# Optimization experiments

Hardware: AMD Instinct MI355X
Metric: run time of the kernel (lower is better)

Reference implementation:

```python
import jax, jax.numpy as jnp
import numpy as np
from jax import lax

B, T, D = 4, 1024, 512      # batch, seq_len, d_model
L = 4                        # n_layers
N = 16                       # d_state
DC = 4                       # d_conv
DI = 2 * D                   # d_inner = expand * d_model
DTR = D // 16                # dt_rank
H = 128                      # head hidden dim
EPS = 1e-5


def layer_norm(x, g, b):
    mu = jnp.mean(x, axis=-1, keepdims=True)
    var = jnp.mean((x - mu) ** 2, axis=-1, keepdims=True)
    return (x - mu) * lax.rsqrt(var + EPS) * g + b


def setup_inputs() -> dict:
    key = jax.random.key(0)
    ks = jax.random.split(key, 24)
    s = 0.02
    return {
        "daily_summaries": jax.random.normal(ks[0], (B, T, D), jnp.float32),
        # per-layer mamba params, stacked on leading L axis
        "in_proj_w": s * jax.random.normal(ks[1], (L, 2 * DI, D), jnp.float32),
        "conv_w": s * jax.random.normal(ks[2], (L, DI, DC), jnp.float32),
        "conv_b": jnp.zeros((L, DI), jnp.float32),
        "x_proj_w": s * jax.random.normal(ks[3], (L, DTR + 2 * N, DI), jnp.float32),
        "dt_proj_w": s * jax.random.normal(ks[4], (L, DI, DTR), jnp.float32),
        "dt_proj_b": jnp.full((L, DI), -4.0, jnp.float32),  # softplus -> small dt
        "A_log": jnp.log(jnp.broadcast_to(jnp.arange(1, N + 1, dtype=jnp.float32), (L, DI, N))),
        "D_skip": jnp.ones((L, DI), jnp.float32),
        "out_proj_w": s * jax.random.normal(ks[5], (L, D, DI), jnp.float32),
        "ln_g": jnp.ones((L, D), jnp.float32),
        "ln_b": jnp.zeros((L, D), jnp.float32),
        # attention pooling
        "attn_w": s * jax.random.normal(ks[6], (1, D), jnp.float32),
        "attn_b": jnp.zeros((1,), jnp.float32),
        # VIX head
        "h1_w": s * jax.random.normal(ks[7], (H, D), jnp.float32),
        "h1_b": jnp.zeros((H,), jnp.float32),
        "ln1_g": jnp.ones((H,), jnp.float32),
        "ln1_b": jnp.zeros((H,), jnp.float32),
        "h2_w": s * jax.random.normal(ks[8], (H, H), jnp.float32),
        "h2_b": jnp.zeros((H,), jnp.float32),
        "ln2_g": jnp.ones((H,), jnp.float32),
        "ln2_b": jnp.zeros((H,), jnp.float32),
        # note: torch zero-inits the final layer; we use random so grads are nonzero
        "h3_w": s * jax.random.normal(ks[9], (1, H), jnp.float32),
        "h3_b": jnp.zeros((1,), jnp.float32),
    }


def mamba_layer(x, in_w, cw, cb, xp_w, dt_w, dt_b, A_log, D_skip, out_w):
    """x: [B,T,D] -> [B,T,D]; canonical Mamba selective scan."""
    xz = jnp.einsum('btd,ed->bte', x, in_w)          # [B,T,2*DI]
    x_in, z = jnp.split(xz, 2, axis=-1)
    # causal depthwise conv over time
    xc = lax.conv_general_dilated(
        x_in.transpose(0, 2, 1), cw[:, None, :], (1,), [(DC - 1, 0)],
        feature_group_count=DI, dimension_numbers=('NCH', 'OIH', 'NCH'))
    xc = jax.nn.silu(xc + cb[None, :, None]).transpose(0, 2, 1)   # [B,T,DI]
    dbc = jnp.einsum('btd,ed->bte', xc, xp_w)        # [B,T,DTR+2N]
    dt_r, Bm, Cm = dbc[..., :DTR], dbc[..., DTR:DTR + N], dbc[..., DTR + N:]
    dt = jax.nn.softplus(jnp.einsum('btr,dr->btd', dt_r, dt_w) + dt_b)  # [B,T,DI]
    A = -jnp.exp(A_log)                              # [DI,N]
    dA = jnp.exp(dt[..., None] * A)                  # [B,T,DI,N]
    dBx = dt[..., None] * Bm[:, :, None, :] * xc[..., None]  # [B,T,DI,N]

    def step(h, inp):
        dA_t, dBx_t, C_t = inp
        h = dA_t * h + dBx_t                         # [B,DI,N]
        return h, jnp.einsum('bdn,bn->bd', h, C_t)

    h0 = jnp.zeros((x.shape[0], DI, N), x.dtype)
    _, ys = lax.scan(step, h0, (dA.transpose(1, 0, 2, 3),
                                dBx.transpose(1, 0, 2, 3),
                                Cm.transpose(1, 0, 2)))
    y = ys.transpose(1, 0, 2) + xc * D_skip          # [B,T,DI]
    y = y * jax.nn.silu(z)
    return jnp.einsum('btd,ed->bte', y, out_w)       # [B,T,D]


def reference(daily_summaries, in_proj_w, conv_w, conv_b, x_proj_w, dt_proj_w,
              dt_proj_b, A_log, D_skip, out_proj_w, ln_g, ln_b, attn_w, attn_b,
              h1_w, h1_b, ln1_g, ln1_b, h2_w, h2_b, ln2_g, ln2_b, h3_w, h3_b):
    x = daily_summaries  # proj is Identity (d_model_l1 == d_model)
    for l in range(L):
        residual = x
        y = mamba_layer(x, in_proj_w[l], conv_w[l], conv_b[l], x_proj_w[l],
                        dt_proj_w[l], dt_proj_b[l], A_log[l], D_skip[l], out_proj_w[l])
        x = layer_norm(y, ln_g[l], ln_b[l]) + residual
    # attention pooling (no mask)
    scores = jnp.einsum('btd,od->bto', x, attn_w) + attn_b   # [B,T,1]
    w = jax.nn.softmax(scores, axis=1)
    pooled = jnp.sum(w * x, axis=1)                          # [B,D]
    # VIX head: Linear -> LN -> GELU (x2) -> Linear
    h1 = jax.nn.gelu(layer_norm(pooled @ h1_w.T + h1_b, ln1_g, ln1_b), approximate=False)
    h2 = jax.nn.gelu(layer_norm(h1 @ h2_w.T + h2_b, ln2_g, ln2_b), approximate=False)
    return (h2 @ h3_w.T + h3_b).squeeze(-1)                  # [B]
```

## Files before the change

### kernel.cpp

```cpp
#include <hip/hip_runtime.h>
#include <hip/hip_bf16.h>
#include <math.h>

#define BATCH 4
#define TLEN 1024
#define DMODEL 512
#define DINNER 1024
#define NSTATE 16
#define EPSV 1e-5f
#define NC 32
#define CT 32
#define DSTR 36
#define LOG2E 1.44269504088896f

typedef __attribute__((ext_vector_type(8))) short bf16x8;
typedef __attribute__((ext_vector_type(4))) float f32x4;

__device__ inline unsigned short f2bf(float f) {
  union { float f; unsigned int u; } c; c.f = f;
  unsigned int u = c.u;
  return (unsigned short)((u + 0x7FFFu + ((u >> 16) & 1u)) >> 16);
}
__device__ inline float bf2f(unsigned short u) {
  union { unsigned int i; float f; } c;
  c.i = ((unsigned int)u) << 16;
  return c.f;
}

__device__ inline float warpReduceSum(float v) {
#pragma unroll
  for (int o = 32; o > 0; o >>= 1) v += __shfl_down(v, o, 64);
  return v;
}
__device__ inline float warpReduceMax(float v) {
#pragma unroll
  for (int o = 32; o > 0; o >>= 1) v = fmaxf(v, __shfl_down(v, o, 64));
  return v;
}
__device__ inline float2 blockReduceSum2_256(float a, float b) {
  __shared__ float sma[4], smb[4];
  int lane = threadIdx.x & 63, wid = threadIdx.x >> 6;
#pragma unroll
  for (int o = 32; o > 0; o >>= 1) { a += __shfl_down(a, o, 64); b += __shfl_down(b, o, 64); }
  if (lane == 0) { sma[wid] = a; smb[wid] = b; }
  __syncthreads();
  float ra = sma[0] + sma[1] + sma[2] + sma[3];
  float rb = smb[0] + smb[1] + smb[2] + smb[3];
  __syncthreads();
  return make_float2(ra, rb);
}
__device__ inline float blockReduceSum256(float v) {
  __shared__ float sm[4];
  int lane = threadIdx.x & 63, wid = threadIdx.x >> 6;
  v = warpReduceSum(v);
  if (lane == 0) sm[wid] = v;
  __syncthreads();
  float r = sm[0] + sm[1] + sm[2] + sm[3];
  __syncthreads();
  return r;
}
__device__ inline float blockReduceMax256(float v) {
  __shared__ float sm[4];
  int lane = threadIdx.x & 63, wid = threadIdx.x >> 6;
  v = warpReduceMax(v);
  if (lane == 0) sm[wid] = v;
  __syncthreads();
  float r = fmaxf(fmaxf(sm[0], sm[1]), fmaxf(sm[2], sm[3]));
  __syncthreads();
  return r;
}
__device__ inline float blockReduceSum128(float v) {
  __shared__ float sm[2];
  int lane = threadIdx.x & 63, wid = threadIdx.x >> 6;
  v = warpReduceSum(v);
  if (lane == 0) sm[wid] = v;
  __syncthreads();
  float r = sm[0] + sm[1];
  __syncthreads();
  return r;
}

__global__ void __launch_bounds__(256)
cast_f32_bf16(const float* __restrict__ src, unsigned short* __restrict__ dst, int n) {
  int i = (blockIdx.x * 256 + threadIdx.x) * 4;
  if (i >= n) return;
  float4 v = *(const float4*)(src + i);
  dst[i + 0] = f2bf(v.x);
  dst[i + 1] = f2bf(v.y);
  dst[i + 2] = f2bf(v.z);
  dst[i + 3] = f2bf(v.w);
}

#define LDP 72
__global__ void __launch_bounds__(256)
gemm_bf16_split(const unsigned short* __restrict__ A, int lda,
                const unsigned short* __restrict__ B, int ldb,
                float* __restrict__ Cx, unsigned short* __restrict__ Cz, int K) {
  __shared__ unsigned short As[128 * LDP];
  __shared__ unsigned short Bs[128 * LDP];
  const int tid = threadIdx.x;
  const int lane = tid & 63, wid = tid >> 6;
  const int wm = wid >> 1, wn = wid & 1;
  const int row0 = blockIdx.y * 128, col0 = blockIdx.x * 128;
  const int c8 = (tid & 7) * 8;
  const int r0 = tid >> 3;
  const int l15 = lane & 15, lq = lane >> 4;
  f32x4 acc[4][4] = {};
  for (int k0 = 0; k0 < K; k0 += 64) {
#pragma unroll
    for (int p = 0; p < 4; p++) {
      int row = r0 + p * 32;
      bf16x8 av = *(const bf16x8*)(A + (size_t)(row0 + row) * lda + k0 + c8);
      bf16x8 bv = *(const bf16x8*)(B + (size_t)(col0 + row) * ldb + k0 + c8);
      *(bf16x8*)(As + row * LDP + c8) = av;
      *(bf16x8*)(Bs + row * LDP + c8) = bv;
    }
    __syncthreads();
#pragma unroll
    for (int s = 0; s < 2; s++) {
      const int koff = s * 32 + lq * 8;
      bf16x8 af[4], bfr[4];
#pragma unroll
      for (int i = 0; i < 4; i++)
        af[i] = *(const bf16x8*)(As + (wm * 64 + i * 16 + l15) * LDP + koff);
#pragma unroll
      for (int j = 0; j < 4; j++)
        bfr[j] = *(const bf16x8*)(Bs + (wn * 64 + j * 16 + l15) * LDP + koff);
#pragma unroll
      for (int i = 0; i < 4; i++)
#pragma unroll
        for (int j = 0; j < 4; j++)
          acc[i][j] = __builtin_amdgcn_mfma_f32_16x16x32_bf16(af[i], bfr[j], acc[i][j], 0, 0, 0);
    }
    __syncthreads();
  }
  if (col0 < 1024) {
#pragma unroll
    for (int i = 0; i < 4; i++)
#pragma unroll
      for (int j = 0; j < 4; j++)
#pragma unroll
        for (int r = 0; r < 4; r++) {
          int row = row0 + wm * 64 + i * 16 + lq * 4 + r;
          int col = col0 + wn * 64 + j * 16 + l15;
          Cx[(size_t)row * 1024 + col] = acc[i][j][r];
        }
  } else {
#pragma unroll
    for (int i = 0; i < 4; i++)
#pragma unroll
      for (int j = 0; j < 4; j++)
#pragma unroll
        for (int r = 0; r < 4; r++) {
          int row = row0 + wm * 64 + i * 16 + lq * 4 + r;
          int col = col0 - 1024 + wn * 64 + j * 16 + l15;
          Cz[(size_t)row * 1024 + col] = f2bf(acc[i][j][r]);
        }
  }
}

__global__ void __launch_bounds__(256)
gemm_bf16_n64(const unsigned short* __restrict__ A, int lda,
              const unsigned short* __restrict__ B, int ldb,
              float* __restrict__ C, int ldc, int K) {
  __shared__ unsigned short As[128 * LDP];
  __shared__ unsigned short Bs[64 * LDP];
  const int tid = threadIdx.x;
  const int lane = tid & 63, wid = tid >> 6;
  const int wm = wid >> 1, wn = wid & 1;
  const int row0 = blockIdx.y * 128, col0 = blockIdx.x * 64;
  const int c8 = (tid & 7) * 8;
  const int r0 = tid >> 3;
  const int l15 = lane & 15, lq = lane >> 4;
  f32x4 acc[4][2] = {};
  for (int k0 = 0; k0 < K; k0 += 64) {
#pragma unroll
    for (int p = 0; p < 4; p++) {
      int row = r0 + p * 32;
      bf16x8 av = *(const bf16x8*)(A + (size_t)(row0 + row) * lda + k0 + c8);
      *(bf16x8*)(As + row * LDP + c8) = av;
    }
#pragma unroll
    for (int p = 0; p < 2; p++) {
      int row = r0 + p * 32;
      bf16x8 bv = *(const bf16x8*)(B + (size_t)(col0 + row) * ldb + k0 + c8);
      *(bf16x8*)(Bs + row * LDP + c8) = bv;
    }
    __syncthreads();
#pragma unroll
    for (int s = 0; s < 2; s++) {
      const int koff = s * 32 + lq * 8;
      bf16x8 af[4], bfr[2];
#pragma unroll
      for (int i = 0; i < 4; i++)
        af[i] = *(const bf16x8*)(As + (wm * 64 + i * 16 + l15) * LDP + koff);
#pragma unroll
      for (int j = 0; j < 2; j++)
        bfr[j] = *(const bf16x8*)(Bs + (wn * 32 + j * 16 + l15) * LDP + koff);
#pragma unroll
      for (int i = 0; i < 4; i++)
#pragma unroll
        for (int j = 0; j < 2; j++)
          acc[i][j] = __builtin_amdgcn_mfma_f32_16x16x32_bf16(af[i], bfr[j], acc[i][j], 0, 0, 0);
    }
    __syncthreads();
  }
#pragma unroll
  for (int i = 0; i < 4; i++)
#pragma unroll
    for (int j = 0; j < 2; j++)
#pragma unroll
      for (int r = 0; r < 4; r++) {
        int row = row0 + wm * 64 + i * 16 + lq * 4 + r;
        int col = col0 + wn * 32 + j * 16 + l15;
        C[(size_t)row * ldc + col] = acc[i][j][r];
      }
}

__global__ void __launch_bounds__(256)
gemm_dt(const float* __restrict__ A, const float* __restrict__ B,
        unsigned short* __restrict__ C, const float* __restrict__ bias) {
  __shared__ __align__(16) float As[16][68];
  __shared__ __align__(16) float Bs[16][68];
  const int tid = threadIdx.x;
  const int tx = tid & 15, ty = tid >> 4;
  const int row0 = blockIdx.y * 64, col0 = blockIdx.x * 64;
  float acc[4][4] = {};
  for (int k0 = 0; k0 < 32; k0 += 16) {
#pragma unroll
    for (int i = 0; i < 4; i++) {
      int e = tid + i * 256;
      int m = e >> 4, kk = e & 15;
      As[kk][m] = A[(size_t)(row0 + m) * 64 + k0 + kk];
      Bs[kk][m] = B[(size_t)(col0 + m) * 32 + k0 + kk];
    }
    __syncthreads();
#pragma unroll
    for (int kk = 0; kk < 16; kk++) {
      float4 a4 = *(const float4*)&As[kk][ty << 2];
      float4 b4 = *(const float4*)&Bs[kk][tx << 2];
      float a[4] = {a4.x, a4.y, a4.z, a4.w};
      float b[4] = {b4.x, b4.y, b4.z, b4.w};
#pragma unroll
      for (int i = 0; i < 4; i++)
#pragma unroll
        for (int j = 0; j < 4; j++) acc[i][j] = fmaf(a[i], b[j], acc[i][j]);
    }
    __syncthreads();
  }
#pragma unroll
  for (int i = 0; i < 4; i++) {
    size_t r = row0 + (ty << 2) + i;
#pragma unroll
    for (int j = 0; j < 4; j++) {
      int c = col0 + (tx << 2) + j;
      float v = acc[i][j] + bias[c];
      v = (v > 20.f) ? v : log1pf(__expf(v));
      C[r * 1024 + c] = f2bf(v);
    }
  }
}

__global__ void conv_silu_kernel(const float* __restrict__ xin,
                                 const float* __restrict__ cw,
                                 const float* __restrict__ cb,
                                 unsigned short* __restrict__ xcbf) {
  int idx = blockIdx.x * 256 + threadIdx.x;
  int d = idx & 1023;
  int bt = idx >> 10;
  int t = bt & 1023;
  float acc = cb[d];
  const float* w = cw + d * 4;
#pragma unroll
  for (int k = 0; k < 4; k++) {
    int ts = t - 3 + k;
    if (ts >= 0) acc = fmaf(xin[((size_t)bt + (ts - t)) * 1024 + d], w[k], acc);
  }
  float sig = 1.f / (1.f + __expf(-acc));
  xcbf[idx] = f2bf(acc * sig);
}

__global__ void __launch_bounds__(256)
scan_part1(const unsigned short* __restrict__ dtbf, const unsigned short* __restrict__ xcbf,
           const float* __restrict__ dbc, const float* __restrict__ A_log,
           float* __restrict__ hloc, float* __restrict__ sdtb) {
  __shared__ unsigned short dts[64 * DSTR];
  __shared__ unsigned short xcs[64 * DSTR];
  __shared__ float Bsh[CT * 20];
  const int chunk = blockIdx.x, dg = blockIdx.y, b = blockIdx.z;
  const int tid = threadIdx.x;
  const int ch = tid >> 2, q4 = (tid & 3) * 4;
  const int d = dg * 64 + ch;
  const size_t bt0 = (size_t)b * TLEN + chunk * CT;
  for (int i = tid; i < CT * 64; i += 256) {
    int t = i >> 6, c = i & 63;
    size_t bt = bt0 + t;
    dts[c * DSTR + t] = dtbf[bt * 1024 + dg * 64 + c];
    xcs[c * DSTR + t] = xcbf[bt * 1024 + dg * 64 + c];
  }
  for (int i = tid; i < CT * 16; i += 256) {
    int t = i >> 4, n = i & 15;
    Bsh[t * 20 + n] = dbc[(bt0 + t) * 64 + 32 + n];
  }
  __syncthreads();
  float4 al = *(const float4*)&A_log[d * 16 + q4];
  float4 A;
  A.x = -__expf(al.x) * LOG2E; A.y = -__expf(al.y) * LOG2E;
  A.z = -__expf(al.z) * LOG2E; A.w = -__expf(al.w) * LOG2E;
  float4 h = {0.f, 0.f, 0.f, 0.f};
  float sdt = 0.f;
#pragma unroll
  for (int t0 = 0; t0 < CT; t0 += 4) {
    ushort4 d4 = *(const ushort4*)&dts[ch * DSTR + t0];
    ushort4 x4 = *(const ushort4*)&xcs[ch * DSTR + t0];
    const float dta[4] = {bf2f(d4.x), bf2f(d4.y), bf2f(d4.z), bf2f(d4.w)};
    const float xca[4] = {bf2f(x4.x), bf2f(x4.y), bf2f(x4.z), bf2f(x4.w)};
#pragma unroll
    for (int u = 0; u < 4; u++) {
      float dtv = dta[u];
      float4 B4 = *(const float4*)&Bsh[(t0 + u) * 20 + q4];
      float uin = dtv * xca[u];
      h.x = fmaf(exp2f(dtv * A.x), h.x, uin * B4.x);
      h.y = fmaf(exp2f(dtv * A.y), h.y, uin * B4.y);
      h.z = fmaf(exp2f(dtv * A.z), h.z, uin * B4.z);
      h.w = fmaf(exp2f(dtv * A.w), h.w, uin * B4.w);
      sdt += dtv;
    }
  }
  size_t slab = (size_t)(b * 16 + dg);
  *(float4*)&hloc[(slab * NC + chunk) * 1024 + tid * 4] = h;
  sdtb[(slab * NC + chunk) * 256 + tid] = sdt;
}

__global__ void __launch_bounds__(256)
scan_prefix(const float* __restrict__ A_log, const float* __restrict__ hloc,
            const float* __restrict__ sdtb, float* __restrict__ h0buf) {
  const int slab = blockIdx.x;
  const int tid = threadIdx.x;
  const int dg = slab & 15;
  const int ch = tid >> 2, q4 = (tid & 3) * 4;
  const int d = dg * 64 + ch;
  float4 al = *(const float4*)&A_log[d * 16 + q4];
  float4 A;
  A.x = -__expf(al.x) * LOG2E; A.y = -__expf(al.y) * LOG2E;
  A.z = -__expf(al.z) * LOG2E; A.w = -__expf(al.w) * LOG2E;
  float4 h = {0.f, 0.f, 0.f, 0.f};
  size_t base = (size_t)slab * NC;
  for (int c = 0; c < NC; c++) {
    *(float4*)&h0buf[(base + c) * 1024 + tid * 4] = h;
    float4 hl = *(const float4*)&hloc[(base + c) * 1024 + tid * 4];
    float s = sdtb[(base + c) * 256 + tid];
    h.x = fmaf(exp2f(s * A.x), h.x, hl.x);
    h.y = fmaf(exp2f(s * A.y), h.y, hl.y);
    h.z = fmaf(exp2f(s * A.z), h.z, hl.z);
    h.w = fmaf(exp2f(s * A.w), h.w, hl.w);
  }
}

__global__ void __launch_bounds__(256)
scan_part2(const unsigned short* __restrict__ dtbf, const unsigned short* __restrict__ xcbf,
           const float* __restrict__ dbc, const unsigned short* __restrict__ zbf,
           const float* __restrict__ A_log, const float* __restrict__ Dsk,
           const float* __restrict__ h0buf, unsigned short* __restrict__ ybf) {
  __shared__ unsigned short dts[64 * DSTR];
  __shared__ unsigned short xcs[64 * DSTR];
  __shared__ float Bsh[CT * 20];
  __shared__ float Csh[CT * 20];
  __shared__ float ys[CT * 64];
  const int chunk = blockIdx.x, dg = blockIdx.y, b = blockIdx.z;
  const int tid = threadIdx.x;
  const int q = tid & 3;
  const int ch = tid >> 2, q4 = q * 4;
  const int d = dg * 64 + ch;
  const size_t bt0 = (size_t)b * TLEN + chunk * CT;
  const size_t slab = (size_t)(b * 16 + dg);
  float4 h = *(const float4*)&h0buf[(slab * NC + chunk) * 1024 + tid * 4];
  float4 al = *(const float4*)&A_log[d * 16 + q4];
  float4 A;
  A.x = -__expf(al.x) * LOG2E; A.y = -__expf(al.y) * LOG2E;
  A.z = -__expf(al.z) * LOG2E; A.w = -__expf(al.w) * LOG2E;
  for (int i = tid; i < CT * 64; i += 256) {
    int t = i >> 6, c = i & 63;
    size_t bt = bt0 + t;
    dts[c * DSTR + t] = dtbf[bt * 1024 + dg * 64 + c];
    xcs[c * DSTR + t] = xcbf[bt * 1024 + dg * 64 + c];
  }
  for (int i = tid; i < CT * 16; i += 256) {
    int t = i >> 4, n = i & 15;
    Bsh[t * 20 + n] = dbc[(bt0 + t) * 64 + 32 + n];
    Csh[t * 20 + n] = dbc[(bt0 + t) * 64 + 48 + n];
  }
  __syncthreads();
  const float Dv = Dsk[d];
#pragma unroll
  for (int t0 = 0; t0 < CT; t0 += 4) {
    ushort4 d4 = *(const ushort4*)&dts[ch * DSTR + t0];
    ushort4 x4 = *(const ushort4*)&xcs[ch * DSTR + t0];
    const float dta[4] = {bf2f(d4.x), bf2f(d4.y), bf2f(d4.z), bf2f(d4.w)};
    const float xca[4] = {bf2f(x4.x), bf2f(x4.y), bf2f(x4.z), bf2f(x4.w)};
#pragma unroll
    for (int u = 0; u < 4; u++) {
      float dtv = dta[u];
      float4 B4 = *(const float4*)&Bsh[(t0 + u) * 20 + q4];
      float4 C4 = *(const float4*)&Csh[(t0 + u) * 20 + q4];
      float uin = dtv * xca[u];
      h.x = fmaf(exp2f(dtv * A.x), h.x, uin * B4.x);
      h.y = fmaf(exp2f(dtv * A.y), h.y, uin * B4.y);
      h.z = fmaf(exp2f(dtv * A.z), h.z, uin * B4.z);
      h.w = fmaf(exp2f(dtv * A.w), h.w, uin * B4.w);
      float cs = h.x * C4.x + h.y * C4.y + h.z * C4.z + h.w * C4.w;
      cs += __shfl_xor(cs, 1, 4);
      cs += __shfl_xor(cs, 2, 4);
      if (q == 0) ys[(t0 + u) * 64 + ch] = cs + xca[u] * Dv;
    }
  }
  __syncthreads();
  for (int i = tid; i < CT * 64; i += 256) {
    int t = i >> 6, c = i & 63;
    size_t bt = bt0 + t;
    float zv = bf2f(zbf[bt * 1024 + dg * 64 + c]);
    float sig = 1.f / (1.f + __expf(-zv));
    ybf[bt * 1024 + dg * 64 + c] = f2bf(ys[t * 64 + c] * (zv * sig));
  }
}

__global__ void __launch_bounds__(256)
ln_res_kernel(const float* __restrict__ mo, const float* __restrict__ res,
              const float* __restrict__ g, const float* __restrict__ bb,
              float* __restrict__ xout, unsigned short* __restrict__ xout_bf) {
  int row = blockIdx.x;
  int tid = threadIdx.x;
  size_t base = (size_t)row * 512;
  float v0 = mo[base + tid], v1 = mo[base + tid + 256];
  float2 ss = blockReduceSum2_256(v0 + v1, v0 * v0 + v1 * v1);
  float mu = ss.x * (1.f / 512.f);
  float var = ss.y * (1.f / 512.f) - mu * mu;
  float rs = rsqrtf(var + EPSV);
  float o0 = (v0 - mu) * rs * g[tid] + bb[tid] + res[base + tid];
  float o1 = (v1 - mu) * rs * g[tid + 256] + bb[tid + 256] + res[base + tid + 256];
  xout[base + tid] = o0;
  xout[base + tid + 256] = o1;
  xout_bf[base + tid] = f2bf(o0);
  xout_bf[base + tid + 256] = f2bf(o1);
}

__global__ void __launch_bounds__(256)
score_kernel(const float* __restrict__ x, const float* __restrict__ aw,
             const float* __restrict__ ab, float* __restrict__ sc) {
  int row = blockIdx.x * 4 + (threadIdx.x >> 6);
  int lane = threadIdx.x & 63;
  size_t base = (size_t)row * 512;
  float p = 0.f;
#pragma unroll
  for (int j = 0; j < 8; j++) p = fmaf(x[base + lane + 64 * j], aw[lane + 64 * j], p);
  p = warpReduceSum(p);
  if (lane == 0) sc[row] = p + ab[0];
}

__global__ void __launch_bounds__(256)
softmax_t_kernel(const float* __restrict__ sc, float* __restrict__ wsm) {
  int b = blockIdx.x, tid = threadIdx.x;
  float v[4];
  float m = -INFINITY;
#pragma unroll
  for (int j = 0; j < 4; j++) { v[j] = sc[b * 1024 + tid + 256 * j]; m = fmaxf(m, v[j]); }
  m = blockReduceMax256(m);
  float s = 0.f;
#pragma unroll
  for (int j = 0; j < 4; j++) { v[j] = __expf(v[j] - m); s += v[j]; }
  s = blockReduceSum256(s);
  float inv = 1.f / s;
#pragma unroll
  for (int j = 0; j < 4; j++) wsm[b * 1024 + tid + 256 * j] = v[j] * inv;
}

__global__ void __launch_bounds__(256)
pool_partial(const float* __restrict__ x, const float* __restrict__ wsm,
             float* __restrict__ partial) {
  int tc = blockIdx.x, b = blockIdx.y, tid = threadIdx.x;
  float a0 = 0.f, a1 = 0.f;
  for (int t = tc * 32; t < tc * 32 + 32; t++) {
    float wv = wsm[b * 1024 + t];
    size_t base = ((size_t)b * 1024 + t) * 512;
    a0 = fmaf(wv, x[base + tid], a0);
    a1 = fmaf(wv, x[base + tid + 256], a1);
  }
  size_t pb = ((size_t)b * 32 + tc) * 512;
  partial[pb + tid] = a0;
  partial[pb + tid + 256] = a1;
}

__global__ void __launch_bounds__(256)
pool_reduce(const float* __restrict__ partial, float* __restrict__ pooled) {
  int b = blockIdx.x, tid = threadIdx.x;
  float a0 = 0.f, a1 = 0.f;
  for (int tc = 0; tc < 32; tc++) {
    size_t pb = ((size_t)b * 32 + tc) * 512;
    a0 += partial[pb + tid];
    a1 += partial[pb + tid + 256];
  }
  pooled[b * 512 + tid] = a0;
  pooled[b * 512 + tid + 256] = a1;
}

__device__ inline float gelu_exact(float x) {
  return 0.5f * x * (1.f + erff(x * 0.70710678118654752f));
}
__global__ void __launch_bounds__(128)
head_kernel(const float* __restrict__ pooled,
            const float* __restrict__ h1w, const float* __restrict__ h1b,
            const float* __restrict__ g1, const float* __restrict__ b1,
            const float* __restrict__ h2w, const float* __restrict__ h2b,
            const float* __restrict__ g2, const float* __restrict__ b2,
            const float* __restrict__ h3w, const float* __restrict__ h3b,
            float* __restrict__ out) {
  int tid = threadIdx.x;
  int b = blockIdx.x;
  __shared__ float hs[128];
  float s = h1b[tid];
  const float* p = pooled + b * 512;
  for (int d = 0; d < 512; d += 4) {
    float4 pv = *(const float4*)(p + d);
    float4 wv = *(const float4*)(h1w + tid * 512 + d);
    s = fmaf(pv.x, wv.x, s); s = fmaf(pv.y, wv.y, s);
    s = fmaf(pv.z, wv.z, s); s = fmaf(pv.w, wv.w, s);
  }
  float mu = blockReduceSum128(s) * (1.f / 128.f);
  float dd = s - mu;
  float var = blockReduceSum128(dd * dd) * (1.f / 128.f);
  float v = dd * rsqrtf(var + EPSV) * g1[tid] + b1[tid];
  hs[tid] = gelu_exact(v);
  __syncthreads();
  float s2 = h2b[tid];
  for (int j = 0; j < 128; j++) s2 = fmaf(hs[j], h2w[tid * 128 + j], s2);
  float mu2 = blockReduceSum128(s2) * (1.f / 128.f);
  float d2 = s2 - mu2;
  float var2 = blockReduceSum128(d2 * d2) * (1.f / 128.f);
  float v2 = d2 * rsqrtf(var2 + EPSV) * g2[tid] + b2[tid];
  float h2v = gelu_exact(v2);
  float o = blockReduceSum128(h2v * h3w[tid]);
  if (tid == 0) out[b] = o + h3b[0];
}

extern "C" void kernel_launch(void* const* d_in, const int* in_sizes, int n_in,
                              void* d_out, int out_size, void* d_ws, size_t ws_size,
                              hipStream_t stream) {
  (void)in_sizes; (void)n_in; (void)out_size; (void)ws_size;
  const float* x0   = (const float*)d_in[0];
  const float* inw  = (const float*)d_in[1];
  const float* cw   = (const float*)d_in[2];
  const float* cb   = (const float*)d_in[3];
  const float* xpw  = (const float*)d_in[4];
  const float* dtw  = (const float*)d_in[5];
  const float* dtb  = (const float*)d_in[6];
  const float* alog = (const float*)d_in[7];
  const float* dsk  = (const float*)d_in[8];
  const float* outw = (const float*)d_in[9];
  const float* lng  = (const float*)d_in[10];
  const float* lnb  = (const float*)d_in[11];
  const float* aw   = (const float*)d_in[12];
  const float* ab   = (const float*)d_in[13];
  const float* h1w  = (const float*)d_in[14];
  const float* h1b  = (const float*)d_in[15];
  const float* g1   = (const float*)d_in[16];
  const float* b1   = (const float*)d_in[17];
  const float* h2w  = (const float*)d_in[18];
  const float* h2b  = (const float*)d_in[19];
  const float* g2   = (const float*)d_in[20];
  const float* b2   = (const float*)d_in[21];
  const float* h3w  = (const float*)d_in[22];
  const float* h3b  = (const float*)d_in[23];

  float* ws = (float*)d_ws;
  float* xin     = ws;
  unsigned short* zbf  = (unsigned short*)(xin + 4194304);
  unsigned short* xcbf = zbf + 4194304;
  unsigned short* dtbf = xcbf + 4194304;
  float* dbc     = (float*)(dtbf + 4194304);
  float* mo      = dbc + 262144;
  float* xbuf    = mo + 2097152;
  float* hloc    = xbuf + 2097152;
  float* sdtb    = hloc + 2097152;
  float* h0buf   = sdtb + 524288;
  float* scores  = h0buf + 2097152;
  float* wsm     = scores + 4096;
  float* partial = wsm + 4096;
  float* pooled  = partial + 65536;
  unsigned short* abuf    = (unsigned short*)(pooled + 2048);
  unsigned short* ybf     = abuf + 2097152;
  unsigned short* wbf_in  = ybf + 4194304;
  unsigned short* wbf_out = wbf_in + 4194304;
  unsigned short* wbf_xp  = wbf_out + 2097152;

  cast_f32_bf16<<<4096, 256, 0, stream>>>(inw, wbf_in, 4194304);
  cast_f32_bf16<<<2048, 256, 0, stream>>>(outw, wbf_out, 2097152);
  cast_f32_bf16<<<256, 256, 0, stream>>>(xpw, wbf_xp, 262144);
  cast_f32_bf16<<<2048, 256, 0, stream>>>(x0, abuf, 2097152);

  const float* xcur = x0;
  for (int l = 0; l < 4; l++) {
    gemm_bf16_split<<<dim3(16, 32), 256, 0, stream>>>(
        abuf, 512, wbf_in + (size_t)l * 2048 * 512, 512, xin, zbf, 512);
    conv_silu_kernel<<<16384, 256, 0, stream>>>(xin, cw + l * 4096, cb + l * 1024, xcbf);
    gemm_bf16_n64<<<dim3(1, 32), 256, 0, stream>>>(
        xcbf, 1024, wbf_xp + (size_t)l * 65536, 1024, dbc, 64, 1024);
    gemm_dt<<<dim3(16, 64), 256, 0, stream>>>(
        dbc, dtw + (size_t)l * 32768, dtbf, dtb + l * 1024);
    scan_part1<<<dim3(NC, 16, 4), 256, 0, stream>>>(
        dtbf, xcbf, dbc, alog + (size_t)l * 16384, hloc, sdtb);
    scan_prefix<<<64, 256, 0, stream>>>(alog + (size_t)l * 16384, hloc, sdtb, h0buf);
    scan_part2<<<dim3(NC, 16, 4), 256, 0, stream>>>(
        dtbf, xcbf, dbc, zbf, alog + (size_t)l * 16384, dsk + l * 1024, h0buf, ybf);
    gemm_bf16_n64<<<dim3(8, 32), 256, 0, stream>>>(
        ybf, 1024, wbf_out + (size_t)l * 524288, 1024, mo, 512, 1024);
    ln_res_kernel<<<4096, 256, 0, stream>>>(mo, xcur, lng + l * 512, lnb + l * 512,
                                            xbuf, abuf);
    xcur = xbuf;
  }
  score_kernel<<<1024, 256, 0, stream>>>(xbuf, aw, ab, scores);
  softmax_t_kernel<<<4, 256, 0, stream>>>(scores, wsm);
  pool_partial<<<dim3(32, 4), 256, 0, stream>>>(xbuf, wsm, partial);
  pool_reduce<<<4, 256, 0, stream>>>(partial, pooled);
  head_kernel<<<4, 128, 0, stream>>>(pooled, h1w, h1b, g1, b1, h2w, h2b, g2, b2,
                                     h3w, h3b, (float*)d_out);
}
```

Measured before the change: 787.4 us.

## Store in_proj x-half as bf16, split-K the x_proj GEMM, pool from bf16 activations

The in_proj GEMM now writes its x half as bf16 instead of fp32, which halves the traffic for that write and for the conv read. The x_proj GEMM, which previously launched only 32 blocks, is split four ways along K into 128 blocks, and a separate reduce kernel sums the fp32 partials. Attention scoring and pooling read the bf16 copy of the final activations instead of fp32. The trade-offs are an extra kernel launch, partial-sum traffic, and lower precision for the conv input and the pooling input.

```diff
diff --git a/kernel.cpp b/kernel.cpp
--- a/kernel.cpp
+++ b/kernel.cpp
@@ -95,7 +95,7 @@
 __global__ void __launch_bounds__(256)
 gemm_bf16_split(const unsigned short* __restrict__ A, int lda,
                 const unsigned short* __restrict__ B, int ldb,
-                float* __restrict__ Cx, unsigned short* __restrict__ Cz, int K) {
+                unsigned short* __restrict__ Cx, unsigned short* __restrict__ Cz, int K) {
   __shared__ unsigned short As[128 * LDP];
   __shared__ unsigned short Bs[128 * LDP];
   const int tid = threadIdx.x;
@@ -134,29 +134,18 @@
     }
     __syncthreads();
   }
-  if (col0 < 1024) {
-#pragma unroll
-    for (int i = 0; i < 4; i++)
-#pragma unroll
-      for (int j = 0; j < 4; j++)
-#pragma unroll
-        for (int r = 0; r < 4; r++) {
-          int row = row0 + wm * 64 + i * 16 + lq * 4 + r;
-          int col = col0 + wn * 64 + j * 16 + l15;
-          Cx[(size_t)row * 1024 + col] = acc[i][j][r];
-        }
-  } else {
-#pragma unroll
-    for (int i = 0; i < 4; i++)
-#pragma unroll
-      for (int j = 0; j < 4; j++)
-#pragma unroll
-        for (int r = 0; r < 4; r++) {
-          int row = row0 + wm * 64 + i * 16 + lq * 4 + r;
-          int col = col0 - 1024 + wn * 64 + j * 16 + l15;
-          Cz[(size_t)row * 1024 + col] = f2bf(acc[i][j][r]);
-        }
-  }
+  unsigned short* dst = (col0 < 1024) ? Cx : Cz;
+  const int cb = (col0 < 1024) ? col0 : (col0 - 1024);
+#pragma unroll
+  for (int i = 0; i < 4; i++)
+#pragma unroll
+    for (int j = 0; j < 4; j++)
+#pragma unroll
+      for (int r = 0; r < 4; r++) {
+        int row = row0 + wm * 64 + i * 16 + lq * 4 + r;
+        int col = cb + wn * 64 + j * 16 + l15;
+        dst[(size_t)row * 1024 + col] = f2bf(acc[i][j][r]);
+      }
 }
 
 __global__ void __launch_bounds__(256)
@@ -218,6 +207,82 @@
 }
 
 __global__ void __launch_bounds__(256)
+gemm_bf16_n64_sk(const unsigned short* __restrict__ A, int lda,
+                 const unsigned short* __restrict__ B, int ldb,
+                 float* __restrict__ Cpart, int KCH) {
+  __shared__ unsigned short As[128 * LDP];
+  __shared__ unsigned short Bs[64 * LDP];
+  const int tid = threadIdx.x;
+  const int lane = tid & 63, wid = tid >> 6;
+  const int wm = wid >> 1, wn = wid & 1;
+  const int row0 = blockIdx.y * 128, col0 = 0;
+  const int kbase = blockIdx.z * KCH;
+  float* Cz = Cpart + (size_t)blockIdx.z * 4096 * 64;
+  const int c8 = (tid & 7) * 8;
+  const int r0 = tid >> 3;
+  const int l15 = lane & 15, lq = lane >> 4;
+  f32x4 acc[4][2] = {};
+  for (int k0 = 0; k0 < KCH; k0 += 64) {
+#pragma unroll
+    for (int p = 0; p < 4; p++) {
+      int row = r0 + p * 32;
+      bf16x8 av = *(const bf16x8*)(A + (size_t)(row0 + row) * lda + kbase + k0 + c8);
+      *(bf16x8*)(As + row * LDP + c8) = av;
+    }
+#pragma unroll
+    for (int p = 0; p < 2; p++) {
+      int row = r0 + p * 32;
+      bf16x8 bv = *(const bf16x8*)(B + (size_t)(col0 + row) * ldb + kbase + k0 + c8);
+      *(bf16x8*)(Bs + row * LDP + c8) = bv;
+    }
+    __syncthreads();
+#pragma unroll
+    for (int s = 0; s < 2; s++) {
+      const int koff = s * 32 + lq * 8;
+      bf16x8 af[4], bfr[2];
+#pragma unroll
+      for (int i = 0; i < 4; i++)
+        af[i] = *(const bf16x8*)(As + (wm * 64 + i * 16 + l15) * LDP + koff);
+#pragma unroll
+      for (int j = 0; j < 2; j++)
+        bfr[j] = *(const bf16x8*)(Bs + (wn * 32 + j * 16 + l15) * LDP + koff);
+#pragma unroll
+      for (int i = 0; i < 4; i++)
+#pragma unroll
+        for (int j = 0; j < 2; j++)
+          acc[i][j] = __builtin_amdgcn_mfma_f32_16x16x32_bf16(af[i], bfr[j], acc[i][j], 0, 0, 0);
+    }
+    __syncthreads();
+  }
+#pragma unroll
+  for (int i = 0; i < 4; i++)
+#pragma unroll
+    for (int j = 0; j < 2; j++)
+#pragma unroll
+      for (int r = 0; r < 4; r++) {
+        int row = row0 + wm * 64 + i * 16 + lq * 4 + r;
+        int col = wn * 32 + j * 16 + l15;
+        Cz[(size_t)row * 64 + col] = acc[i][j][r];
+      }
+}
+
+__global__ void __launch_bounds__(256)
+reduce4_kernel(const float* __restrict__ part, float* __restrict__ out, int n) {
+  int i = (blockIdx.x * 256 + threadIdx.x) * 4;
+  if (i >= n) return;
+  float4 a = *(const float4*)(part + i);
+  float4 b = *(const float4*)(part + n + i);
+  float4 c = *(const float4*)(part + 2 * n + i);
+  float4 d = *(const float4*)(part + 3 * n + i);
+  float4 r;
+  r.x = a.x + b.x + c.x + d.x;
+  r.y = a.y + b.y + c.y + d.y;
+  r.z = a.z + b.z + c.z + d.z;
+  r.w = a.w + b.w + c.w + d.w;
+  *(float4*)(out + i) = r;
+}
+
+__global__ void __launch_bounds__(256)
 gemm_dt(const float* __restrict__ A, const float* __restrict__ B,
         unsigned short* __restrict__ C, const float* __restrict__ bias) {
   __shared__ __align__(16) float As[16][68];
@@ -261,7 +326,7 @@
   }
 }
 
-__global__ void conv_silu_kernel(const float* __restrict__ xin,
+__global__ void conv_silu_kernel(const unsigned short* __restrict__ xinbf,
                                  const float* __restrict__ cw,
                                  const float* __restrict__ cb,
                                  unsigned short* __restrict__ xcbf) {
@@ -274,7 +339,7 @@
 #pragma unroll
   for (int k = 0; k < 4; k++) {
     int ts = t - 3 + k;
-    if (ts >= 0) acc = fmaf(xin[((size_t)bt + (ts - t)) * 1024 + d], w[k], acc);
+    if (ts >= 0) acc = fmaf(bf2f(xinbf[((size_t)bt + (ts - t)) * 1024 + d]), w[k], acc);
   }
   float sig = 1.f / (1.f + __expf(-acc));
   xcbf[idx] = f2bf(acc * sig);
@@ -445,14 +510,15 @@
 }
 
 __global__ void __launch_bounds__(256)
-score_kernel(const float* __restrict__ x, const float* __restrict__ aw,
+score_kernel(const unsigned short* __restrict__ x, const float* __restrict__ aw,
              const float* __restrict__ ab, float* __restrict__ sc) {
   int row = blockIdx.x * 4 + (threadIdx.x >> 6);
   int lane = threadIdx.x & 63;
   size_t base = (size_t)row * 512;
   float p = 0.f;
 #pragma unroll
-  for (int j = 0; j < 8; j++) p = fmaf(x[base + lane + 64 * j], aw[lane + 64 * j], p);
+  for (int j = 0; j < 8; j++)
+    p = fmaf(bf2f(x[base + lane + 64 * j]), aw[lane + 64 * j], p);
   p = warpReduceSum(p);
   if (lane == 0) sc[row] = p + ab[0];
 }
@@ -475,15 +541,15 @@
 }
 
 __global__ void __launch_bounds__(256)
-pool_partial(const float* __restrict__ x, const float* __restrict__ wsm,
+pool_partial(const unsigned short* __restrict__ x, const float* __restrict__ wsm,
              float* __restrict__ partial) {
   int tc = blockIdx.x, b = blockIdx.y, tid = threadIdx.x;
   float a0 = 0.f, a1 = 0.f;
   for (int t = tc * 32; t < tc * 32 + 32; t++) {
     float wv = wsm[b * 1024 + t];
     size_t base = ((size_t)b * 1024 + t) * 512;
-    a0 = fmaf(wv, x[base + tid], a0);
-    a1 = fmaf(wv, x[base + tid + 256], a1);
+    a0 = fmaf(wv, bf2f(x[base + tid]), a0);
+    a1 = fmaf(wv, bf2f(x[base + tid + 256]), a1);
   }
   size_t pb = ((size_t)b * 32 + tc) * 512;
   partial[pb + tid] = a0;
@@ -572,12 +638,13 @@
   const float* h3b  = (const float*)d_in[23];
 
   float* ws = (float*)d_ws;
-  float* xin     = ws;
-  unsigned short* zbf  = (unsigned short*)(xin + 4194304);
-  unsigned short* xcbf = zbf + 4194304;
-  unsigned short* dtbf = xcbf + 4194304;
+  unsigned short* xinbf = (unsigned short*)ws;
+  unsigned short* zbf   = xinbf + 4194304;
+  unsigned short* xcbf  = zbf + 4194304;
+  unsigned short* dtbf  = xcbf + 4194304;
   float* dbc     = (float*)(dtbf + 4194304);
-  float* mo      = dbc + 262144;
+  float* xpart   = dbc + 262144;
+  float* mo      = xpart + 1048576;
   float* xbuf    = mo + 2097152;
   float* hloc    = xbuf + 2097152;
   float* sdtb    = hloc + 2097152;
@@ -600,10 +667,11 @@
   const float* xcur = x0;
   for (int l = 0; l < 4; l++) {
     gemm_bf16_split<<<dim3(16, 32), 256, 0, stream>>>(
-        abuf, 512, wbf_in + (size_t)l * 2048 * 512, 512, xin, zbf, 512);
-    conv_silu_kernel<<<16384, 256, 0, stream>>>(xin, cw + l * 4096, cb + l * 1024, xcbf);
-    gemm_bf16_n64<<<dim3(1, 32), 256, 0, stream>>>(
-        xcbf, 1024, wbf_xp + (size_t)l * 65536, 1024, dbc, 64, 1024);
+        abuf, 512, wbf_in + (size_t)l * 2048 * 512, 512, xinbf, zbf, 512);
+    conv_silu_kernel<<<16384, 256, 0, stream>>>(xinbf, cw + l * 4096, cb + l * 1024, xcbf);
+    gemm_bf16_n64_sk<<<dim3(1, 32, 4), 256, 0, stream>>>(
+        xcbf, 1024, wbf_xp + (size_t)l * 65536, 1024, xpart, 256);
+    reduce4_kernel<<<256, 256, 0, stream>>>(xpart, dbc, 262144);
     gemm_dt<<<dim3(16, 64), 256, 0, stream>>>(
         dbc, dtw + (size_t)l * 32768, dtbf, dtb + l * 1024);
     scan_part1<<<dim3(NC, 16, 4), 256, 0, stream>>>(
@@ -617,9 +685,9 @@
                                             xbuf, abuf);
     xcur = xbuf;
   }
-  score_kernel<<<1024, 256, 0, stream>>>(xbuf, aw, ab, scores);
+  score_kernel<<<1024, 256, 0, stream>>>(abuf, aw, ab, scores);
   softmax_t_kernel<<<4, 256, 0, stream>>>(scores, wsm);
-  pool_partial<<<dim3(32, 4), 256, 0, stream>>>(xbuf, wsm, partial);
+  pool_partial<<<dim3(32, 4), 256, 0, stream>>>(abuf, wsm, partial);
   pool_reduce<<<4, 256, 0, stream>>>(partial, pooled);
   head_kernel<<<4, 128, 0, stream>>>(pooled, h1w, h1b, g1, b1, h2w, h2b, g2, b2,
                                      h3w, h3b, (float*)d_out);
```

Result: faster. 762.2 us (-3.2%).
